# Kernel optimization log

Measured on AMD Instinct MI355X. Metric: run time of the kernel, lower is better.

## Reference

```python
import jax, jax.numpy as jnp
import numpy as np

N, E = 50000, 1600000
IN_DIM, EMBED, OUT = 512, 128, 64


def setup_inputs() -> dict:
    key = jax.random.key(0)
    k = jax.random.split(key, 8)
    x = jax.random.normal(k[0], (N, IN_DIM), dtype=jnp.float32)
    edge_index = jax.random.randint(k[1], (2, E), 0, N, dtype=jnp.int32)
    W_dense = jax.random.normal(k[2], (EMBED, IN_DIM), dtype=jnp.float32) * 0.02
    b_dense = jnp.zeros((EMBED,), dtype=jnp.float32)
    W_gat = jax.random.normal(k[3], (OUT, EMBED), dtype=jnp.float32) * 0.05
    att_src = jax.random.normal(k[4], (OUT,), dtype=jnp.float32) * 0.1
    att_dst = jax.random.normal(k[5], (OUT,), dtype=jnp.float32) * 0.1
    b_gat = jnp.zeros((OUT,), dtype=jnp.float32)
    return {"x": x, "edge_index": edge_index, "W_dense": W_dense, "b_dense": b_dense,
            "W_gat": W_gat, "att_src": att_src, "att_dst": att_dst, "b_gat": b_gat}


def reference(x, edge_index, W_dense, b_dense, W_gat, att_src, att_dst, b_gat):
    # dense -> LeakyReLU(0.01) (nn.LeakyReLU default)
    h = jax.nn.leaky_relu(x @ W_dense.T + b_dense, negative_slope=0.01)  # [N, EMBED]
    n = h.shape[0]
    # GATConv (PyG, heads=1, add_self_loops=True, negative_slope=0.2)
    loops = jnp.arange(n, dtype=edge_index.dtype)
    src = jnp.concatenate([edge_index[0], loops])
    dst = jnp.concatenate([edge_index[1], loops])
    g = h @ W_gat.T  # [N, OUT]
    a_src = g @ att_src  # [N]
    a_dst = g @ att_dst  # [N]
    e = jax.nn.leaky_relu(a_src[src] + a_dst[dst], negative_slope=0.2)  # [E+N]
    # segment softmax over destination neighborhoods (self loops guarantee non-empty)
    m = jax.ops.segment_max(e, dst, num_segments=n)
    e = jnp.exp(e - m[dst])
    denom = jax.ops.segment_sum(e, dst, num_segments=n)
    alpha = e / denom[dst]
    out = jax.ops.segment_sum(g[src] * alpha[:, None], dst, num_segments=n) + b_gat
    # original returns ([embed_x], [embed_x]); we return the single embedding tensor
    return out
```

## Files before the change

kernel.cpp:

```cpp
#include <hip/hip_runtime.h>
#include <math.h>

#define IN_DIM 512
#define EMBED 128
#define OUT_DIM 64
#define NBPAD 256
#define SEGSH 12
#define CAP_LDS 10240

typedef __attribute__((ext_vector_type(8))) short bf16x8;
typedef __attribute__((ext_vector_type(4))) float f32x4;

__device__ __forceinline__ float lrelu(float v, float s) { return v > 0.f ? v : v * s; }

__device__ __forceinline__ float readlane_f(float v, int l) {
  return __int_as_float(__builtin_amdgcn_readlane(__float_as_int(v), l));
}

__device__ __forceinline__ unsigned short f2bf(float f) {
  unsigned int u = __float_as_uint(f);
  u += 0x7fff + ((u >> 16) & 1);
  return (unsigned short)(u >> 16);
}
__device__ __forceinline__ float bf2f(unsigned short h) {
  return __uint_as_float(((unsigned int)h) << 16);
}

__device__ __forceinline__ unsigned int cvt_pk_bf16(float a, float b) {
  unsigned int r;
  asm("v_cvt_pk_bf16_f32 %0, %1, %2" : "=v"(r) : "v"(a), "v"(b));
  return r;
}

__device__ __forceinline__ void gl_lds16(const void* g, void* l) {
  __builtin_amdgcn_global_load_lds(
      (const __attribute__((address_space(1))) unsigned int*)g,
      (__attribute__((address_space(3))) unsigned int*)l, 16, 0, 0);
}

#define LDA 40

__global__ __launch_bounds__(256) void split_w_kernel(
    const float* __restrict__ W, unsigned short* __restrict__ Wh,
    unsigned short* __restrict__ Wl, int total) {
  int i = (blockIdx.x * 256 + threadIdx.x) * 4;
  if (i >= total) return;
  float4 v = *(const float4*)(W + i);
  unsigned int h0 = cvt_pk_bf16(v.x, v.y);
  unsigned int h1 = cvt_pk_bf16(v.z, v.w);
  float r0 = v.x - __uint_as_float(h0 << 16);
  float r1 = v.y - __uint_as_float(h0 & 0xffff0000u);
  float r2 = v.z - __uint_as_float(h1 << 16);
  float r3 = v.w - __uint_as_float(h1 & 0xffff0000u);
  unsigned int l0 = cvt_pk_bf16(r0, r1);
  unsigned int l1 = cvt_pk_bf16(r2, r3);
  uint2 hh = make_uint2(h0, h1);
  uint2 ll = make_uint2(l0, l1);
  *(uint2*)(Wh + i) = hh;
  *(uint2*)(Wl + i) = ll;
}

__global__ __launch_bounds__(256) void gemm1_mfma_kernel(
    const float* __restrict__ x, const unsigned short* __restrict__ Wdh,
    const unsigned short* __restrict__ Wdl, const float* __restrict__ bd,
    float* __restrict__ h, int N) {
  __shared__ __align__(16) unsigned char Bhs[2][8192];
  __shared__ __align__(16) unsigned char Bls[2][8192];

  const int tid = threadIdx.x;
  const int lane = tid & 63;
  const int wid = tid >> 6;
  const int mblk = blockIdx.x * 128;
  const int quad = lane >> 4;
  const int l15 = lane & 15;

  const float* aptr[2];
#pragma unroll
  for (int mi = 0; mi < 2; ++mi) {
    int rg = mblk + wid * 32 + mi * 16 + l15;
    if (rg >= N) rg = N - 1;
    aptr[mi] = x + (size_t)rg * IN_DIM + quad * 8;
  }
  float4 tc[2][2];
  auto loadA = [&](int k0) {
#pragma unroll
    for (int mi = 0; mi < 2; ++mi) {
      tc[mi][0] = *(const float4*)(aptr[mi] + k0);
      tc[mi][1] = *(const float4*)(aptr[mi] + k0 + 4);
    }
  };

  const char* bsrcH[2];
  const char* bsrcL[2];
  int bdst[2];
#pragma unroll
  for (int i = 0; i < 2; ++i) {
    int chunk = i * 256 + tid;
    int row = chunk >> 2, ch = chunk & 3;
    int cs = ch ^ ((row >> 1) & 3);
    size_t srcoff = (size_t)row * (IN_DIM * 2) + (cs << 4);
    bsrcH[i] = (const char*)Wdh + srcoff;
    bsrcL[i] = (const char*)Wdl + srcoff;
    bdst[i] = chunk * 16;
  }
  auto stageB = [&](int buf, int k0) {
    const size_t kb = (size_t)k0 * 2;
#pragma unroll
    for (int i = 0; i < 2; ++i) {
      gl_lds16(bsrcH[i] + kb, Bhs[buf] + bdst[i]);
      gl_lds16(bsrcL[i] + kb, Bls[buf] + bdst[i]);
    }
  };

  int boff[8];
#pragma unroll
  for (int ni = 0; ni < 8; ++ni) {
    int row = ni * 16 + l15;
    boff[ni] = row * 64 + ((quad ^ ((row >> 1) & 3)) << 4);
  }

  f32x4 acc[2][8];
#pragma unroll
  for (int i = 0; i < 2; ++i)
#pragma unroll
    for (int j = 0; j < 8; ++j) acc[i][j] = (f32x4){0.f, 0.f, 0.f, 0.f};

  stageB(0, 0);
  loadA(0);
  __syncthreads();

#pragma unroll 2
  for (int s = 0; s < IN_DIM / 32; ++s) {
    const int buf = s & 1;
    if (s + 1 < IN_DIM / 32) stageB(buf ^ 1, (s + 1) * 32);

    bf16x8 AH[2], AL[2];
#pragma unroll
    for (int mi = 0; mi < 2; ++mi) {
      float av[8] = {tc[mi][0].x, tc[mi][0].y, tc[mi][0].z, tc[mi][0].w,
                     tc[mi][1].x, tc[mi][1].y, tc[mi][1].z, tc[mi][1].w};
      union { unsigned int u[4]; bf16x8 v; } H, L;
#pragma unroll
      for (int i = 0; i < 4; ++i) {
        unsigned int hp = cvt_pk_bf16(av[2 * i], av[2 * i + 1]);
        float q0 = av[2 * i] - __uint_as_float(hp << 16);
        float q1 = av[2 * i + 1] - __uint_as_float(hp & 0xffff0000u);
        H.u[i] = hp;
        L.u[i] = cvt_pk_bf16(q0, q1);
      }
      AH[mi] = H.v;
      AL[mi] = L.v;
    }
    if (s + 1 < IN_DIM / 32) loadA((s + 1) * 32);

#pragma unroll
    for (int hf = 0; hf < 2; ++hf) {
      bf16x8 BH[4], BL[4];
#pragma unroll
      for (int j = 0; j < 4; ++j) {
        BH[j] = *(const bf16x8*)(Bhs[buf] + boff[hf * 4 + j]);
        BL[j] = *(const bf16x8*)(Bls[buf] + boff[hf * 4 + j]);
      }
#pragma unroll
      for (int mi = 0; mi < 2; ++mi)
#pragma unroll
        for (int j = 0; j < 4; ++j) {
          int ni = hf * 4 + j;
          acc[mi][ni] = __builtin_amdgcn_mfma_f32_16x16x32_bf16(AH[mi], BH[j], acc[mi][ni], 0, 0, 0);
          acc[mi][ni] = __builtin_amdgcn_mfma_f32_16x16x32_bf16(AL[mi], BH[j], acc[mi][ni], 0, 0, 0);
          acc[mi][ni] = __builtin_amdgcn_mfma_f32_16x16x32_bf16(AH[mi], BL[j], acc[mi][ni], 0, 0, 0);
        }
    }
    __syncthreads();
  }

#pragma unroll
  for (int mi = 0; mi < 2; ++mi)
#pragma unroll
    for (int ni = 0; ni < 8; ++ni) {
      int n = ni * 16 + l15;
      float b = bd[n];
#pragma unroll
      for (int r = 0; r < 4; ++r) {
        int m = mblk + wid * 32 + mi * 16 + quad * 4 + r;
        if (m < N) h[(size_t)m * EMBED + n] = lrelu(acc[mi][ni][r] + b, 0.01f);
      }
    }
}

__global__ __launch_bounds__(256) void gemm2_mfma_kernel(
    const float* __restrict__ h, const float* __restrict__ Wg,
    const float* __restrict__ att_src, const float* __restrict__ att_dst,
    float* __restrict__ g, float* __restrict__ a_src, float* __restrict__ a_dst,
    int N) {
  __shared__ __align__(16) unsigned short Ah[128][LDA];
  __shared__ __align__(16) unsigned short Al[128][LDA];
  __shared__ __align__(16) unsigned short Bh[64][LDA];
  __shared__ __align__(16) unsigned short Bl[64][LDA];

  const int tid = threadIdx.x;
  const int lane = tid & 63;
  const int wid = tid >> 6;
  const int wr = wid >> 1, wc = wid & 1;
  const int mblk = blockIdx.x * 128;
  const int quad = lane >> 4;
  const int l15 = lane & 15;

  const int arow = tid >> 1, acb = (tid & 1) * 16;
  const int brow = tid >> 2, bcb = (tid & 3) * 8;
  const bool avalid = (mblk + arow) < N;
  const float* aptr = h + (size_t)(mblk + arow) * EMBED + acb;
  const float* bptr = Wg + (size_t)brow * EMBED + bcb;

  f32x4 acc[4][2];
#pragma unroll
  for (int i = 0; i < 4; ++i)
#pragma unroll
    for (int j = 0; j < 2; ++j) acc[i][j] = (f32x4){0.f, 0.f, 0.f, 0.f};

  float4 t0, t1, t2, t3, u0, u1;
  auto do_load = [&](int k0) {
    if (avalid) {
      t0 = *(const float4*)(aptr + k0);
      t1 = *(const float4*)(aptr + k0 + 4);
      t2 = *(const float4*)(aptr + k0 + 8);
      t3 = *(const float4*)(aptr + k0 + 12);
    } else {
      t0 = t1 = t2 = t3 = make_float4(0.f, 0.f, 0.f, 0.f);
    }
    u0 = *(const float4*)(bptr + k0);
    u1 = *(const float4*)(bptr + k0 + 4);
  };
  do_load(0);

  for (int k0 = 0; k0 < EMBED; k0 += 32) {
    float av[16] = {t0.x, t0.y, t0.z, t0.w, t1.x, t1.y, t1.z, t1.w,
                    t2.x, t2.y, t2.z, t2.w, t3.x, t3.y, t3.z, t3.w};
    union { unsigned short us[16]; uint4 v[2]; } AH, AL;
#pragma unroll
    for (int i = 0; i < 16; ++i) {
      unsigned short hi = f2bf(av[i]);
      AH.us[i] = hi;
      AL.us[i] = f2bf(av[i] - bf2f(hi));
    }
    float bv[8] = {u0.x, u0.y, u0.z, u0.w, u1.x, u1.y, u1.z, u1.w};
    union { unsigned short us[8]; uint4 v; } BH, BL;
#pragma unroll
    for (int i = 0; i < 8; ++i) {
      unsigned short hi = f2bf(bv[i]);
      BH.us[i] = hi;
      BL.us[i] = f2bf(bv[i] - bf2f(hi));
    }

    __syncthreads();
    *(uint4*)&Ah[arow][acb] = AH.v[0];
    *(uint4*)&Ah[arow][acb + 8] = AH.v[1];
    *(uint4*)&Al[arow][acb] = AL.v[0];
    *(uint4*)&Al[arow][acb + 8] = AL.v[1];
    *(uint4*)&Bh[brow][bcb] = BH.v;
    *(uint4*)&Bl[brow][bcb] = BL.v;
    __syncthreads();

    if (k0 + 32 < EMBED) do_load(k0 + 32);

    bf16x8 ah[4], al[4], bh[2], bl[2];
#pragma unroll
    for (int mi = 0; mi < 4; ++mi) {
      int r = wr * 64 + mi * 16 + l15;
      ah[mi] = *(const bf16x8*)&Ah[r][quad * 8];
      al[mi] = *(const bf16x8*)&Al[r][quad * 8];
    }
#pragma unroll
    for (int ni = 0; ni < 2; ++ni) {
      int r = wc * 32 + ni * 16 + l15;
      bh[ni] = *(const bf16x8*)&Bh[r][quad * 8];
      bl[ni] = *(const bf16x8*)&Bl[r][quad * 8];
    }
#pragma unroll
    for (int mi = 0; mi < 4; ++mi)
#pragma unroll
      for (int ni = 0; ni < 2; ++ni) {
        acc[mi][ni] = __builtin_amdgcn_mfma_f32_16x16x32_bf16(ah[mi], bh[ni], acc[mi][ni], 0, 0, 0);
        acc[mi][ni] = __builtin_amdgcn_mfma_f32_16x16x32_bf16(al[mi], bh[ni], acc[mi][ni], 0, 0, 0);
        acc[mi][ni] = __builtin_amdgcn_mfma_f32_16x16x32_bf16(ah[mi], bl[ni], acc[mi][ni], 0, 0, 0);
      }
  }

  float as_[2], ad_[2];
#pragma unroll
  for (int ni = 0; ni < 2; ++ni) {
    int n = wc * 32 + ni * 16 + l15;
    as_[ni] = att_src[n];
    ad_[ni] = att_dst[n];
  }
#pragma unroll
  for (int mi = 0; mi < 4; ++mi) {
#pragma unroll
    for (int r = 0; r < 4; ++r) {
      int m = mblk + wr * 64 + mi * 16 + quad * 4 + r;
      float ps = acc[mi][0][r] * as_[0] + acc[mi][1][r] * as_[1];
      float pd = acc[mi][0][r] * ad_[0] + acc[mi][1][r] * ad_[1];
#pragma unroll
      for (int d = 1; d < 16; d <<= 1) {
        ps += __shfl_xor(ps, d, 64);
        pd += __shfl_xor(pd, d, 64);
      }
      if (m < N) {
#pragma unroll
        for (int ni = 0; ni < 2; ++ni) {
          int n = wc * 32 + ni * 16 + l15;
          g[(size_t)m * OUT_DIM + n] = acc[mi][ni][r];
        }
        if (l15 == 0 && wc == 0) {
          a_src[m] = ps;
          a_dst[m] = pd;
        }
      }
    }
  }
  __syncthreads();
#pragma unroll
  for (int mi = 0; mi < 4; ++mi) {
#pragma unroll
    for (int r = 0; r < 4; ++r) {
      int m = mblk + wr * 64 + mi * 16 + quad * 4 + r;
      float ps = acc[mi][0][r] * as_[0] + acc[mi][1][r] * as_[1];
      float pd = acc[mi][0][r] * ad_[0] + acc[mi][1][r] * ad_[1];
#pragma unroll
      for (int d = 1; d < 16; d <<= 1) {
        ps += __shfl_xor(ps, d, 64);
        pd += __shfl_xor(pd, d, 64);
      }
      if (m < N && l15 == 0 && wc == 1) {
        atomicAdd(&a_src[m], ps);
        atomicAdd(&a_dst[m], pd);
      }
    }
  }
}

__global__ __launch_bounds__(256) void hist_count_kernel(
    const int* __restrict__ ei, int* __restrict__ histT, int nblkP, int E,
    int N) {
  __shared__ int cnt[NBPAD];
  const int t = threadIdx.x;
  cnt[t] = 0;
  __syncthreads();
  const int T = E + N;
  const int base = blockIdx.x << SEGSH;
#pragma unroll
  for (int q = 0; q < (1 << SEGSH) / 256; ++q) {
    int i = base + q * 256 + t;
    if (i < T) {
      int d = (i < E) ? ei[E + i] : (i - E);
      atomicAdd(&cnt[d >> 8], 1);
    }
  }
  __syncthreads();
  histT[(size_t)t * nblkP + blockIdx.x] = cnt[t];
}

__global__ __launch_bounds__(256) void row_scan_kernel(
    int* __restrict__ histT, int* __restrict__ bucket_tot, int nblkP) {
  __shared__ int sc[256];
  const int t = threadIdx.x;
  int* row = histT + (size_t)blockIdx.x * nblkP;
  const int per = (nblkP + 255) / 256;
  int loc[8];
  int sum = 0;
#pragma unroll 4
  for (int j = 0; j < per; ++j) {
    int idx = t * per + j;
    int v = (idx < nblkP) ? row[idx] : 0;
    loc[j] = sum;
    sum += v;
  }
  sc[t] = sum;
  __syncthreads();
  for (int dlt = 1; dlt < 256; dlt <<= 1) {
    int add = (t >= dlt) ? sc[t - dlt] : 0;
    __syncthreads();
    sc[t] += add;
    __syncthreads();
  }
  const int off = sc[t] - sum;
#pragma unroll 4
  for (int j = 0; j < per; ++j) {
    int idx = t * per + j;
    if (idx < nblkP) row[idx] = off + loc[j];
  }
  if (t == 255) bucket_tot[blockIdx.x] = sc[255];
}

__global__ __launch_bounds__(256) void base_scan_kernel(
    const int* __restrict__ bucket_tot, int* __restrict__ bucket_base,
    int* __restrict__ offsets, int N, int T) {
  __shared__ int sc[256];
  const int t = threadIdx.x;
  int v = bucket_tot[t];
  sc[t] = v;
  __syncthreads();
  for (int dlt = 1; dlt < 256; dlt <<= 1) {
    int add = (t >= dlt) ? sc[t - dlt] : 0;
    __syncthreads();
    sc[t] += add;
    __syncthreads();
  }
  bucket_base[t] = sc[t] - v;
  if (t == 0) offsets[N] = T;
}

__global__ __launch_bounds__(256) void bin_kernel(
    const int* __restrict__ ei, const int* __restrict__ histT,
    const int* __restrict__ bucket_base, int* __restrict__ stageB, int nblkP,
    int E, int N) {
  __shared__ int cnt[NBPAD];
  __shared__ int basev[NBPAD];
  const int t = threadIdx.x;
  cnt[t] = 0;
  basev[t] = bucket_base[t] + histT[(size_t)t * nblkP + blockIdx.x];
  __syncthreads();
  const int T = E + N;
  const int base = blockIdx.x << SEGSH;
#pragma unroll
  for (int q = 0; q < (1 << SEGSH) / 256; ++q) {
    int i = base + q * 256 + t;
    if (i < T) {
      int s, d;
      if (i < E) {
        s = ei[i];
        d = ei[E + i];
      } else {
        s = d = i - E;
      }
      int b = d >> 8;
      int r = atomicAdd(&cnt[b], 1);
      stageB[basev[b] + r] = (s << 8) | (d & 255);
    }
  }
}

__global__ __launch_bounds__(256) void build_kernel(
    const int* __restrict__ stageB, const int* __restrict__ bucket_base,
    const int* __restrict__ bucket_tot, const float* __restrict__ a_src,
    const float* __restrict__ a_dst, int* __restrict__ offsets,
    int2* __restrict__ csr_pack, int N) {
  __shared__ int cnt[256];
  __shared__ int pre[256];
  __shared__ int cur[256];
  __shared__ int2 buf[CAP_LDS];
  const int b = blockIdx.x;
  const int t = threadIdx.x;
  const int base = bucket_base[b];
  const int tot = bucket_tot[b];
  cnt[t] = 0;
  __syncthreads();
  const int* sp = stageB + base;
  for (int i = t; i < tot; i += 256) atomicAdd(&cnt[sp[i] & 255], 1);
  __syncthreads();
  int v = cnt[t];
  pre[t] = v;
  __syncthreads();
  for (int dlt = 1; dlt < 256; dlt <<= 1) {
    int add = (t >= dlt) ? pre[t - dlt] : 0;
    __syncthreads();
    pre[t] += add;
    __syncthreads();
  }
  const int excl = pre[t] - v;
  cur[t] = excl;
  const int d_self = (b << 8) | t;
  if (d_self < N) offsets[d_self] = base + excl;
  __syncthreads();
  for (int i = t; i < tot; i += 256) {
    int rec = sp[i];
    int dl = rec & 255;
    int s = rec >> 8;
    float e = a_src[s] + a_dst[(b << 8) | dl];
    e = e > 0.f ? e : 0.2f * e;
    int pos = atomicAdd(&cur[dl], 1);
    int2 r2 = make_int2(s, __float_as_int(e));
    if (pos < CAP_LDS)
      buf[pos] = r2;
    else
      csr_pack[base + pos] = r2;
  }
  __syncthreads();
  const int lim = min(tot, CAP_LDS);
  for (int i = t; i < lim; i += 256) csr_pack[base + i] = buf[i];
}

__global__ __launch_bounds__(256) void aggregate_kernel(
    const int* __restrict__ offsets, const int2* __restrict__ csr_pack,
    const float* __restrict__ g, const float* __restrict__ b_gat,
    float* __restrict__ out, int N) {
  const int lane = threadIdx.x & 63;
  const int node = blockIdx.x * 4 + (threadIdx.x >> 6);
  if (node >= N) return;
  const int beg = offsets[node], end = offsets[node + 1];

  float m = -1e30f;
  for (int j = beg + lane; j < end; j += 64)
    m = fmaxf(m, __int_as_float(csr_pack[j].y));
#pragma unroll
  for (int d = 1; d < 64; d <<= 1) m = fmaxf(m, __shfl_xor(m, d, 64));

  float l = 0.f;
  for (int j = beg + lane; j < end; j += 64)
    l += __expf(__int_as_float(csr_pack[j].y) - m);
#pragma unroll
  for (int d = 1; d < 64; d <<= 1) l += __shfl_xor(l, d, 64);
  const float inv_l = 1.f / l;

  float acc0 = 0.f, acc1 = 0.f, acc2 = 0.f, acc3 = 0.f;
  for (int jb = beg; jb < end; jb += 64) {
    int j = jb + lane;
    float p = 0.f;
    int s = 0;
    if (j < end) {
      int2 rec = csr_pack[j];
      p = __expf(__int_as_float(rec.y) - m) * inv_l;
      s = rec.x;
    }
    const int cnt = min(64, end - jb);
    int jj = 0;
    for (; jj + 4 <= cnt; jj += 4) {
      int s0 = __builtin_amdgcn_readlane(s, jj);
      int s1 = __builtin_amdgcn_readlane(s, jj + 1);
      int s2 = __builtin_amdgcn_readlane(s, jj + 2);
      int s3 = __builtin_amdgcn_readlane(s, jj + 3);
      float p0 = readlane_f(p, jj);
      float p1 = readlane_f(p, jj + 1);
      float p2 = readlane_f(p, jj + 2);
      float p3 = readlane_f(p, jj + 3);
      acc0 += p0 * g[((size_t)s0 << 6) + lane];
      acc1 += p1 * g[((size_t)s1 << 6) + lane];
      acc2 += p2 * g[((size_t)s2 << 6) + lane];
      acc3 += p3 * g[((size_t)s3 << 6) + lane];
    }
    for (; jj < cnt; ++jj) {
      int s0 = __builtin_amdgcn_readlane(s, jj);
      float p0 = readlane_f(p, jj);
      acc0 += p0 * g[((size_t)s0 << 6) + lane];
    }
  }
  out[(size_t)node * OUT_DIM + lane] = (acc0 + acc1) + (acc2 + acc3) + b_gat[lane];
}

extern "C" void kernel_launch(void* const* d_in, const int* in_sizes, int n_in,
                              void* d_out, int out_size, void* d_ws, size_t ws_size,
                              hipStream_t stream) {
  const float* x = (const float*)d_in[0];
  const int* ei = (const int*)d_in[1];
  const float* Wd = (const float*)d_in[2];
  const float* bd = (const float*)d_in[3];
  const float* Wg = (const float*)d_in[4];
  const float* att_src = (const float*)d_in[5];
  const float* att_dst = (const float*)d_in[6];
  const float* bg = (const float*)d_in[7];
  float* out = (float*)d_out;

  const int N = in_sizes[0] / IN_DIM;
  const int E = in_sizes[1] / 2;
  const int T = E + N;
  const int NB = (N + 255) >> 8;
  const int nblkP = (T + (1 << SEGSH) - 1) >> SEGSH;

  char* ws = (char*)d_ws;
  size_t off = 0;
  auto alloc = [&](size_t bytes) -> void* {
    void* p = ws + off;
    off += (bytes + 15) & ~(size_t)15;
    return p;
  };
  float* h = (float*)alloc((size_t)N * EMBED * 4);
  float* g = (float*)alloc((size_t)N * OUT_DIM * 4);
  float* a_src = (float*)alloc((size_t)N * 4);
  float* a_dst = (float*)alloc((size_t)N * 4);
  int* offsets = (int*)alloc((size_t)(N + 1) * 4);
  int* histT = (int*)alloc((size_t)NBPAD * nblkP * 4);
  int* bucket_base = (int*)alloc((size_t)NBPAD * 4);
  int* bucket_tot = (int*)alloc((size_t)NBPAD * 4);
  int* stageB = (int*)alloc((size_t)T * 4);
  int2* csr_pack = (int2*)alloc((size_t)T * 8);
  unsigned short* Wdh = (unsigned short*)alloc((size_t)EMBED * IN_DIM * 2);
  unsigned short* Wdl = (unsigned short*)alloc((size_t)EMBED * IN_DIM * 2);

  const int WTOT = EMBED * IN_DIM;
  hipLaunchKernelGGL(split_w_kernel, dim3(WTOT / 1024), dim3(256), 0, stream,
                     Wd, Wdh, Wdl, WTOT);
  hipLaunchKernelGGL(gemm1_mfma_kernel, dim3((N + 127) / 128), dim3(256), 0,
                     stream, x, Wdh, Wdl, bd, h, N);
  hipLaunchKernelGGL(gemm2_mfma_kernel, dim3((N + 127) / 128), dim3(256), 0,
                     stream, h, Wg, att_src, att_dst, g, a_src, a_dst, N);
  hipLaunchKernelGGL(hist_count_kernel, dim3(nblkP), dim3(256), 0, stream,
                     ei, histT, nblkP, E, N);
  hipLaunchKernelGGL(row_scan_kernel, dim3(NBPAD), dim3(256), 0, stream,
                     histT, bucket_tot, nblkP);
  hipLaunchKernelGGL(base_scan_kernel, dim3(1), dim3(256), 0, stream,
                     bucket_tot, bucket_base, offsets, N, T);
  hipLaunchKernelGGL(bin_kernel, dim3(nblkP), dim3(256), 0, stream,
                     ei, histT, bucket_base, stageB, nblkP, E, N);
  hipLaunchKernelGGL(build_kernel, dim3(NB), dim3(256), 0, stream,
                     stageB, bucket_base, bucket_tot, a_src, a_dst, offsets,
                     csr_pack, N);
  hipLaunchKernelGGL(aggregate_kernel, dim3((N + 3) / 4), dim3(256), 0, stream,
                     offsets, csr_pack, g, bg, out, N);
}
```

Baseline: 322.6 us.

## Pre-split h and W_gat into bf16 hi/lo pairs and restructure gemm2

```diff
diff --git a/kernel.cpp b/kernel.cpp
--- a/kernel.cpp
+++ b/kernel.cpp
@@ -41,11 +41,21 @@
 #define LDA 40
 
 __global__ __launch_bounds__(256) void split_w_kernel(
-    const float* __restrict__ W, unsigned short* __restrict__ Wh,
-    unsigned short* __restrict__ Wl, int total) {
+    const float* __restrict__ Wd, unsigned short* __restrict__ Wdh,
+    unsigned short* __restrict__ Wdl, const float* __restrict__ Wg,
+    unsigned short* __restrict__ Wgh, unsigned short* __restrict__ Wgl) {
   int i = (blockIdx.x * 256 + threadIdx.x) * 4;
-  if (i >= total) return;
-  float4 v = *(const float4*)(W + i);
+  const float* W;
+  unsigned short *Wh, *Wl;
+  int base;
+  if (i < EMBED * IN_DIM) {
+    W = Wd; Wh = Wdh; Wl = Wdl; base = i;
+  } else {
+    base = i - EMBED * IN_DIM;
+    if (base >= OUT_DIM * EMBED) return;
+    W = Wg; Wh = Wgh; Wl = Wgl;
+  }
+  float4 v = *(const float4*)(W + base);
   unsigned int h0 = cvt_pk_bf16(v.x, v.y);
   unsigned int h1 = cvt_pk_bf16(v.z, v.w);
   float r0 = v.x - __uint_as_float(h0 << 16);
@@ -54,16 +64,14 @@
   float r3 = v.w - __uint_as_float(h1 & 0xffff0000u);
   unsigned int l0 = cvt_pk_bf16(r0, r1);
   unsigned int l1 = cvt_pk_bf16(r2, r3);
-  uint2 hh = make_uint2(h0, h1);
-  uint2 ll = make_uint2(l0, l1);
-  *(uint2*)(Wh + i) = hh;
-  *(uint2*)(Wl + i) = ll;
+  *(uint2*)(Wh + base) = make_uint2(h0, h1);
+  *(uint2*)(Wl + base) = make_uint2(l0, l1);
 }
 
 __global__ __launch_bounds__(256) void gemm1_mfma_kernel(
     const float* __restrict__ x, const unsigned short* __restrict__ Wdh,
     const unsigned short* __restrict__ Wdl, const float* __restrict__ bd,
-    float* __restrict__ h, int N) {
+    unsigned int* __restrict__ hp, int N) {
   __shared__ __align__(16) unsigned char Bhs[2][8192];
   __shared__ __align__(16) unsigned char Bls[2][8192];
 
@@ -142,10 +150,10 @@
       union { unsigned int u[4]; bf16x8 v; } H, L;
 #pragma unroll
       for (int i = 0; i < 4; ++i) {
-        unsigned int hp = cvt_pk_bf16(av[2 * i], av[2 * i + 1]);
-        float q0 = av[2 * i] - __uint_as_float(hp << 16);
-        float q1 = av[2 * i + 1] - __uint_as_float(hp & 0xffff0000u);
-        H.u[i] = hp;
+        unsigned int hpk = cvt_pk_bf16(av[2 * i], av[2 * i + 1]);
+        float q0 = av[2 * i] - __uint_as_float(hpk << 16);
+        float q1 = av[2 * i + 1] - __uint_as_float(hpk & 0xffff0000u);
+        H.u[i] = hpk;
         L.u[i] = cvt_pk_bf16(q0, q1);
       }
       AH[mi] = H.v;
@@ -183,123 +191,111 @@
 #pragma unroll
       for (int r = 0; r < 4; ++r) {
         int m = mblk + wid * 32 + mi * 16 + quad * 4 + r;
-        if (m < N) h[(size_t)m * EMBED + n] = lrelu(acc[mi][ni][r] + b, 0.01f);
+        float v = lrelu(acc[mi][ni][r] + b, 0.01f);
+        unsigned short hi = f2bf(v);
+        unsigned short lo = f2bf(v - bf2f(hi));
+        if (m < N) hp[(size_t)m * EMBED + n] = ((unsigned int)hi << 16) | lo;
       }
     }
 }
 
 __global__ __launch_bounds__(256) void gemm2_mfma_kernel(
-    const float* __restrict__ h, const float* __restrict__ Wg,
-    const float* __restrict__ att_src, const float* __restrict__ att_dst,
-    float* __restrict__ g, float* __restrict__ a_src, float* __restrict__ a_dst,
-    int N) {
-  __shared__ __align__(16) unsigned short Ah[128][LDA];
-  __shared__ __align__(16) unsigned short Al[128][LDA];
-  __shared__ __align__(16) unsigned short Bh[64][LDA];
-  __shared__ __align__(16) unsigned short Bl[64][LDA];
+    const unsigned int* __restrict__ hp, const unsigned short* __restrict__ Wgh,
+    const unsigned short* __restrict__ Wgl, const float* __restrict__ att_src,
+    const float* __restrict__ att_dst, float* __restrict__ g,
+    float* __restrict__ a_src, float* __restrict__ a_dst, int N) {
+  __shared__ __align__(16) unsigned char Bhs[16384];
+  __shared__ __align__(16) unsigned char Bls[16384];
 
   const int tid = threadIdx.x;
   const int lane = tid & 63;
   const int wid = tid >> 6;
-  const int wr = wid >> 1, wc = wid & 1;
   const int mblk = blockIdx.x * 128;
   const int quad = lane >> 4;
   const int l15 = lane & 15;
 
-  const int arow = tid >> 1, acb = (tid & 1) * 16;
-  const int brow = tid >> 2, bcb = (tid & 3) * 8;
-  const bool avalid = (mblk + arow) < N;
-  const float* aptr = h + (size_t)(mblk + arow) * EMBED + acb;
-  const float* bptr = Wg + (size_t)brow * EMBED + bcb;
-
-  f32x4 acc[4][2];
-#pragma unroll
-  for (int i = 0; i < 4; ++i)
-#pragma unroll
-    for (int j = 0; j < 2; ++j) acc[i][j] = (f32x4){0.f, 0.f, 0.f, 0.f};
-
-  float4 t0, t1, t2, t3, u0, u1;
-  auto do_load = [&](int k0) {
-    if (avalid) {
-      t0 = *(const float4*)(aptr + k0);
-      t1 = *(const float4*)(aptr + k0 + 4);
-      t2 = *(const float4*)(aptr + k0 + 8);
-      t3 = *(const float4*)(aptr + k0 + 12);
-    } else {
-      t0 = t1 = t2 = t3 = make_float4(0.f, 0.f, 0.f, 0.f);
-    }
-    u0 = *(const float4*)(bptr + k0);
-    u1 = *(const float4*)(bptr + k0 + 4);
-  };
-  do_load(0);
-
-  for (int k0 = 0; k0 < EMBED; k0 += 32) {
-    float av[16] = {t0.x, t0.y, t0.z, t0.w, t1.x, t1.y, t1.z, t1.w,
-                    t2.x, t2.y, t2.z, t2.w, t3.x, t3.y, t3.z, t3.w};
-    union { unsigned short us[16]; uint4 v[2]; } AH, AL;
-#pragma unroll
-    for (int i = 0; i < 16; ++i) {
-      unsigned short hi = f2bf(av[i]);
-      AH.us[i] = hi;
-      AL.us[i] = f2bf(av[i] - bf2f(hi));
-    }
-    float bv[8] = {u0.x, u0.y, u0.z, u0.w, u1.x, u1.y, u1.z, u1.w};
-    union { unsigned short us[8]; uint4 v; } BH, BL;
-#pragma unroll
-    for (int i = 0; i < 8; ++i) {
-      unsigned short hi = f2bf(bv[i]);
-      BH.us[i] = hi;
-      BL.us[i] = f2bf(bv[i] - bf2f(hi));
-    }
-
-    __syncthreads();
-    *(uint4*)&Ah[arow][acb] = AH.v[0];
-    *(uint4*)&Ah[arow][acb + 8] = AH.v[1];
-    *(uint4*)&Al[arow][acb] = AL.v[0];
-    *(uint4*)&Al[arow][acb + 8] = AL.v[1];
-    *(uint4*)&Bh[brow][bcb] = BH.v;
-    *(uint4*)&Bl[brow][bcb] = BL.v;
-    __syncthreads();
-
-    if (k0 + 32 < EMBED) do_load(k0 + 32);
-
-    bf16x8 ah[4], al[4], bh[2], bl[2];
-#pragma unroll
-    for (int mi = 0; mi < 4; ++mi) {
-      int r = wr * 64 + mi * 16 + l15;
-      ah[mi] = *(const bf16x8*)&Ah[r][quad * 8];
-      al[mi] = *(const bf16x8*)&Al[r][quad * 8];
-    }
-#pragma unroll
-    for (int ni = 0; ni < 2; ++ni) {
-      int r = wc * 32 + ni * 16 + l15;
-      bh[ni] = *(const bf16x8*)&Bh[r][quad * 8];
-      bl[ni] = *(const bf16x8*)&Bl[r][quad * 8];
-    }
-#pragma unroll
-    for (int mi = 0; mi < 4; ++mi)
-#pragma unroll
-      for (int ni = 0; ni < 2; ++ni) {
-        acc[mi][ni] = __builtin_amdgcn_mfma_f32_16x16x32_bf16(ah[mi], bh[ni], acc[mi][ni], 0, 0, 0);
-        acc[mi][ni] = __builtin_amdgcn_mfma_f32_16x16x32_bf16(al[mi], bh[ni], acc[mi][ni], 0, 0, 0);
-        acc[mi][ni] = __builtin_amdgcn_mfma_f32_16x16x32_bf16(ah[mi], bl[ni], acc[mi][ni], 0, 0, 0);
-      }
-  }
-
-  float as_[2], ad_[2];
-#pragma unroll
-  for (int ni = 0; ni < 2; ++ni) {
-    int n = wc * 32 + ni * 16 + l15;
+  const char* aptr[2];
+#pragma unroll
+  for (int mi = 0; mi < 2; ++mi) {
+    int rg = mblk + wid * 32 + mi * 16 + l15;
+    if (rg >= N) rg = N - 1;
+    aptr[mi] = (const char*)hp + (size_t)rg * (EMBED * 4) + quad * 32;
+  }
+  uint4 areg[2][4][2];
+#pragma unroll
+  for (int mi = 0; mi < 2; ++mi)
+#pragma unroll
+    for (int ks = 0; ks < 4; ++ks) {
+      areg[mi][ks][0] = *(const uint4*)(aptr[mi] + ks * 128);
+      areg[mi][ks][1] = *(const uint4*)(aptr[mi] + ks * 128 + 16);
+    }
+
+#pragma unroll
+  for (int i = 0; i < 4; ++i) {
+    int chunk = i * 256 + tid;
+    int row = chunk >> 4, ch = chunk & 15;
+    size_t srcoff = (size_t)row * (EMBED * 2) + ((ch ^ (row & 15)) << 4);
+    gl_lds16((const char*)Wgh + srcoff, Bhs + chunk * 16);
+    gl_lds16((const char*)Wgl + srcoff, Bls + chunk * 16);
+  }
+  __syncthreads();
+
+  f32x4 acc[2][4];
+#pragma unroll
+  for (int i = 0; i < 2; ++i)
+#pragma unroll
+    for (int j = 0; j < 4; ++j) acc[i][j] = (f32x4){0.f, 0.f, 0.f, 0.f};
+
+#pragma unroll
+  for (int ks = 0; ks < 4; ++ks) {
+    bf16x8 AH[2], AL[2];
+#pragma unroll
+    for (int mi = 0; mi < 2; ++mi) {
+      union { unsigned int u[8]; uint4 v[2]; } W_;
+      W_.v[0] = areg[mi][ks][0];
+      W_.v[1] = areg[mi][ks][1];
+      union { unsigned int u[4]; bf16x8 v; } H, L;
+#pragma unroll
+      for (int p = 0; p < 4; ++p) {
+        unsigned int wA = W_.u[2 * p], wB = W_.u[2 * p + 1];
+        H.u[p] = __builtin_amdgcn_perm(wB, wA, 0x07060302u);
+        L.u[p] = __builtin_amdgcn_perm(wB, wA, 0x05040100u);
+      }
+      AH[mi] = H.v;
+      AL[mi] = L.v;
+    }
+#pragma unroll
+    for (int ni = 0; ni < 4; ++ni) {
+      int row = ni * 16 + l15;
+      int chunk = ks * 4 + quad;
+      int off = row * 256 + (((chunk ^ (row & 15))) << 4);
+      bf16x8 BH = *(const bf16x8*)(Bhs + off);
+      bf16x8 BL = *(const bf16x8*)(Bls + off);
+#pragma unroll
+      for (int mi = 0; mi < 2; ++mi) {
+        acc[mi][ni] = __builtin_amdgcn_mfma_f32_16x16x32_bf16(AH[mi], BH, acc[mi][ni], 0, 0, 0);
+        acc[mi][ni] = __builtin_amdgcn_mfma_f32_16x16x32_bf16(AL[mi], BH, acc[mi][ni], 0, 0, 0);
+        acc[mi][ni] = __builtin_amdgcn_mfma_f32_16x16x32_bf16(AH[mi], BL, acc[mi][ni], 0, 0, 0);
+      }
+    }
+  }
+
+  float as_[4], ad_[4];
+#pragma unroll
+  for (int ni = 0; ni < 4; ++ni) {
+    int n = ni * 16 + l15;
     as_[ni] = att_src[n];
     ad_[ni] = att_dst[n];
   }
 #pragma unroll
-  for (int mi = 0; mi < 4; ++mi) {
+  for (int mi = 0; mi < 2; ++mi) {
 #pragma unroll
     for (int r = 0; r < 4; ++r) {
-      int m = mblk + wr * 64 + mi * 16 + quad * 4 + r;
-      float ps = acc[mi][0][r] * as_[0] + acc[mi][1][r] * as_[1];
-      float pd = acc[mi][0][r] * ad_[0] + acc[mi][1][r] * ad_[1];
+      int m = mblk + wid * 32 + mi * 16 + quad * 4 + r;
+      float ps = acc[mi][0][r] * as_[0] + acc[mi][1][r] * as_[1] +
+                 acc[mi][2][r] * as_[2] + acc[mi][3][r] * as_[3];
+      float pd = acc[mi][0][r] * ad_[0] + acc[mi][1][r] * ad_[1] +
+                 acc[mi][2][r] * ad_[2] + acc[mi][3][r] * ad_[3];
 #pragma unroll
       for (int d = 1; d < 16; d <<= 1) {
         ps += __shfl_xor(ps, d, 64);
@@ -307,33 +303,12 @@
       }
       if (m < N) {
 #pragma unroll
-        for (int ni = 0; ni < 2; ++ni) {
-          int n = wc * 32 + ni * 16 + l15;
-          g[(size_t)m * OUT_DIM + n] = acc[mi][ni][r];
-        }
-        if (l15 == 0 && wc == 0) {
+        for (int ni = 0; ni < 4; ++ni)
+          g[(size_t)m * OUT_DIM + ni * 16 + l15] = acc[mi][ni][r];
+        if (l15 == 0) {
           a_src[m] = ps;
           a_dst[m] = pd;
         }
-      }
-    }
-  }
-  __syncthreads();
-#pragma unroll
-  for (int mi = 0; mi < 4; ++mi) {
-#pragma unroll
-    for (int r = 0; r < 4; ++r) {
-      int m = mblk + wr * 64 + mi * 16 + quad * 4 + r;
-      float ps = acc[mi][0][r] * as_[0] + acc[mi][1][r] * as_[1];
-      float pd = acc[mi][0][r] * ad_[0] + acc[mi][1][r] * ad_[1];
-#pragma unroll
-      for (int d = 1; d < 16; d <<= 1) {
-        ps += __shfl_xor(ps, d, 64);
-        pd += __shfl_xor(pd, d, 64);
-      }
-      if (m < N && l15 == 0 && wc == 1) {
-        atomicAdd(&a_src[m], ps);
-        atomicAdd(&a_dst[m], pd);
       }
     }
   }
@@ -573,7 +548,7 @@
     off += (bytes + 15) & ~(size_t)15;
     return p;
   };
-  float* h = (float*)alloc((size_t)N * EMBED * 4);
+  unsigned int* hpk = (unsigned int*)alloc((size_t)N * EMBED * 4);
   float* g = (float*)alloc((size_t)N * OUT_DIM * 4);
   float* a_src = (float*)alloc((size_t)N * 4);
   float* a_dst = (float*)alloc((size_t)N * 4);
@@ -585,14 +560,16 @@
   int2* csr_pack = (int2*)alloc((size_t)T * 8);
   unsigned short* Wdh = (unsigned short*)alloc((size_t)EMBED * IN_DIM * 2);
   unsigned short* Wdl = (unsigned short*)alloc((size_t)EMBED * IN_DIM * 2);
-
-  const int WTOT = EMBED * IN_DIM;
-  hipLaunchKernelGGL(split_w_kernel, dim3(WTOT / 1024), dim3(256), 0, stream,
-                     Wd, Wdh, Wdl, WTOT);
+  unsigned short* Wgh = (unsigned short*)alloc((size_t)OUT_DIM * EMBED * 2);
+  unsigned short* Wgl = (unsigned short*)alloc((size_t)OUT_DIM * EMBED * 2);
+
+  const int SPLIT_TOT = EMBED * IN_DIM + OUT_DIM * EMBED;
+  hipLaunchKernelGGL(split_w_kernel, dim3(SPLIT_TOT / 1024), dim3(256), 0,
+                     stream, Wd, Wdh, Wdl, Wg, Wgh, Wgl);
   hipLaunchKernelGGL(gemm1_mfma_kernel, dim3((N + 127) / 128), dim3(256), 0,
-                     stream, x, Wdh, Wdl, bd, h, N);
+                     stream, x, Wdh, Wdl, bd, hpk, N);
   hipLaunchKernelGGL(gemm2_mfma_kernel, dim3((N + 127) / 128), dim3(256), 0,
-                     stream, h, Wg, att_src, att_dst, g, a_src, a_dst, N);
+                     stream, hpk, Wgh, Wgl, att_src, att_dst, g, a_src, a_dst, N);
   hipLaunchKernelGGL(hist_count_kernel, dim3(nblkP), dim3(256), 0, stream,
                      ei, histT, nblkP, E, N);
   hipLaunchKernelGGL(row_scan_kernel, dim3(NBPAD), dim3(256), 0, stream,
```

New measurement: 316.6 us. No clear change (-1.9%).
